# Optimization experiments

Hardware: AMD Instinct MI355X
Metric: run time of the kernel (lower is better)

The kernel has to match this reference:

```python
import jax, jax.numpy as jnp
import numpy as np

D_MODEL = 1024
D_STATE = 16
D_CONV = 4
EXPAND = 2
D_INNER = D_MODEL * EXPAND
B = 2
L = 1024


def setup_inputs() -> dict:
    key = jax.random.key(0)
    ks = jax.random.split(key, 8)
    s = lambda k, shape, scale: jax.random.normal(k, shape, dtype=jnp.float32) * scale
    x = s(ks[0], (B, L, D_MODEL), 1.0)
    W_in = s(ks[1], (2 * D_INNER, D_MODEL), D_MODEL ** -0.5)
    conv_w = s(ks[2], (D_INNER, D_CONV), D_CONV ** -0.5)
    conv_b = s(ks[3], (D_INNER,), 0.02)
    W_x = s(ks[4], (2 * D_STATE + 1, D_INNER), D_INNER ** -0.5)
    dt_w = s(ks[5], (D_INNER, 1), 1.0)
    dt_b = s(ks[6], (D_INNER,), 0.02)
    A_log = jnp.log(jnp.broadcast_to(jnp.arange(1, D_STATE + 1, dtype=jnp.float32), (D_INNER, D_STATE)))
    D_param = jnp.ones((D_INNER,), dtype=jnp.float32)
    W_out = s(ks[7], (D_MODEL, D_INNER), D_INNER ** -0.5)
    return dict(x=x, W_in=W_in, conv_w=conv_w, conv_b=conv_b, W_x=W_x,
                dt_w=dt_w, dt_b=dt_b, A_log=A_log, D_param=D_param, W_out=W_out)


def _causal_dwconv(x, w, b):
    # x: (B,L,D), w: (D,K), b: (D,). torch Conv1d(pad=K-1)[..., :L] == left-pad causal conv.
    K = w.shape[1]
    Lx = x.shape[1]
    xp = jnp.pad(x, ((0, 0), (K - 1, 0), (0, 0)))
    return sum(xp[:, k:k + Lx, :] * w[:, k] for k in range(K)) + b


def reference(x, W_in, conv_w, conv_b, W_x, dt_w, dt_b, A_log, D_param, W_out):
    Bb, Ll, _ = x.shape
    xz = jnp.einsum('bld,ed->ble', x, W_in)          # (B,L,2*D_INNER)
    x_ssm, z = jnp.split(xz, 2, axis=-1)
    xc = jax.nn.silu(_causal_dwconv(x_ssm, conv_w, conv_b))  # (B,L,D_INNER)

    proj = jnp.einsum('bld,ed->ble', xc, W_x)        # (B,L,1+2N)
    dt_raw = proj[..., :1]
    B_vals = proj[..., 1:1 + D_STATE]                # (B,L,N)
    C_vals = proj[..., 1 + D_STATE:]                 # (B,L,N)
    dt = jax.nn.softplus(dt_raw * dt_w[:, 0] + dt_b)  # (B,L,D_INNER)

    A = -jnp.exp(A_log)                              # (D_INNER,N)
    dA = jnp.exp(dt[..., None] * A)                  # (B,L,D,N)
    dBx = dt[..., None] * B_vals[:, :, None, :] * xc[..., None]  # (B,L,D,N)

    def step(h, inputs):
        dA_t, dBx_t, C_t = inputs
        h = dA_t * h + dBx_t                         # (B,D,N)
        y_t = jnp.einsum('bdn,bn->bd', h, C_t)
        return h, y_t

    h0 = jnp.zeros((Bb, D_INNER, D_STATE), dtype=x.dtype)
    xs = (jnp.moveaxis(dA, 1, 0), jnp.moveaxis(dBx, 1, 0), jnp.moveaxis(C_vals, 1, 0))
    _, ys = jax.lax.scan(step, h0, xs)               # ys: (L,B,D)
    y = jnp.moveaxis(ys, 0, 1) + xc * D_param        # skip connection
    y = y * jax.nn.silu(z)
    return jnp.einsum('bld,ed->ble', y, W_out)
```

## Files before the change

kernel.cpp:

```cpp
#include <hip/hip_runtime.h>
#include <cstdint>
#include <cstddef>

#define DM 1024
#define DI 2048
#define DS 16
#define LSEQ 1024
#define NROWS 2048
#define CHUNKS 32
#define CLEN 32
#define PSTRIDE 36

typedef __attribute__((ext_vector_type(8))) short short8;
typedef __attribute__((ext_vector_type(4))) float float4v;

__device__ __forceinline__ float bf2f(ushort u) {
  union { float f; uint32_t i; } v; v.i = ((uint32_t)u) << 16; return v.f;
}
__device__ __forceinline__ ushort f2bf(float f) {
  union { float f; uint32_t i; } v; v.f = f;
  uint32_t x = v.i;
  uint32_t r = (x + 0x7fffu + ((x >> 16) & 1u)) >> 16;
  return (ushort)r;
}

__device__ __forceinline__ void gl2lds16(const ushort* g, ushort* l) {
  __builtin_amdgcn_global_load_lds(
      (const __attribute__((address_space(1))) unsigned int*)g,
      (__attribute__((address_space(3))) unsigned int*)l,
      16, 0, 0);
}

#define NX   (NROWS * DM)
#define NWIN (2 * DI * DM)
#define NWOUT (DM * DI)
#define NWX  (33 * DI)

__global__ __launch_bounds__(256)
void cast_all(const float* __restrict__ x, const float* __restrict__ W_in,
              const float* __restrict__ W_out, const float* __restrict__ Wx,
              ushort* __restrict__ xb, ushort* __restrict__ wib,
              ushort* __restrict__ wob, ushort* __restrict__ wxb) {
  int i = (blockIdx.x * 256 + threadIdx.x) * 8;
  const float* src;
  ushort* dst;
  int off;
  if (i < NX) { src = x; dst = xb; off = 0; }
  else if (i < NX + NWIN) { src = W_in; dst = wib; off = NX; }
  else if (i < NX + NWIN + NWOUT) { src = W_out; dst = wob; off = NX + NWIN; }
  else if (i < NX + NWIN + NWOUT + NWX) { src = Wx; dst = wxb; off = NX + NWIN + NWOUT; }
  else return;
  int j = i - off;
  float4v a = *(const float4v*)(src + j);
  float4v b = *(const float4v*)(src + j + 4);
  short8 o;
#pragma unroll
  for (int k = 0; k < 4; ++k) o[k] = (short)f2bf(a[k]);
#pragma unroll
  for (int k = 0; k < 4; ++k) o[4 + k] = (short)f2bf(b[k]);
  *(short8*)(dst + j) = o;
}

template <typename OUT_T>
__global__ __launch_bounds__(256, 2)
void gemm_bt(const ushort* __restrict__ A, const ushort* __restrict__ B,
             OUT_T* __restrict__ C, int M, int N, int K, int lda, int ldb) {
  __shared__ ushort As[128 * 64];
  __shared__ ushort Bs[128 * 64];
  const int tid = threadIdx.x;
  const int wave = tid >> 6;
  const int lane = tid & 63;
  const int m16 = lane & 15;
  const int quad = lane >> 4;
  const int row0 = blockIdx.x * 128;
  const int col0 = blockIdx.y * 128;
  const int wm = (wave >> 1) * 64;
  const int wn = (wave & 1) * 64;

  const ushort *Ap[4], *Bp[4];
  ushort *Asd[4], *Bsd[4];
#pragma unroll
  for (int q = 0; q < 4; ++q) {
    int c = tid + 256 * q;
    Ap[q] = A + (size_t)(row0 + (c >> 3)) * lda + (c & 7) * 8;
    Bp[q] = B + (size_t)(col0 + (c >> 3)) * ldb + (c & 7) * 8;
    Asd[q] = As + c * 8;
    Bsd[q] = Bs + c * 8;
  }

  float4v acc[4][4] = {};

  for (int k0 = 0; k0 < K; k0 += 64) {
    __syncthreads();
#pragma unroll
    for (int q = 0; q < 4; ++q) gl2lds16(Ap[q], Asd[q]);
#pragma unroll
    for (int q = 0; q < 4; ++q) gl2lds16(Bp[q], Bsd[q]);
#pragma unroll
    for (int q = 0; q < 4; ++q) { Ap[q] += 64; Bp[q] += 64; }
    __syncthreads();

#pragma unroll
    for (int kk = 0; kk < 64; kk += 32) {
      short8 af[4], bfr[4];
#pragma unroll
      for (int i = 0; i < 4; ++i)
        af[i] = *(const short8*)&As[(wm + i * 16 + m16) * 64 + kk + quad * 8];
#pragma unroll
      for (int j = 0; j < 4; ++j)
        bfr[j] = *(const short8*)&Bs[(wn + j * 16 + m16) * 64 + kk + quad * 8];
#pragma unroll
      for (int i = 0; i < 4; ++i)
#pragma unroll
        for (int j = 0; j < 4; ++j)
          acc[i][j] = __builtin_amdgcn_mfma_f32_16x16x32_bf16(af[i], bfr[j], acc[i][j], 0, 0, 0);
    }
  }

#pragma unroll
  for (int i = 0; i < 4; ++i) {
#pragma unroll
    for (int r = 0; r < 4; ++r) {
      int row = row0 + wm + i * 16 + quad * 4 + r;
#pragma unroll
      for (int j = 0; j < 4; ++j) {
        int col = col0 + wn + j * 16 + m16;
        float v = acc[i][j][r];
        if constexpr (sizeof(OUT_T) == 4)
          C[(size_t)row * N + col] = v;
        else
          C[(size_t)row * N + col] = f2bf(v);
      }
    }
  }
}

__global__ __launch_bounds__(256, 2)
void gemm_bt64(const ushort* __restrict__ A, const ushort* __restrict__ B,
               float* __restrict__ C, int M, int N, int K, int lda, int ldb) {
  __shared__ ushort As[64 * 32];
  __shared__ ushort Bs[64 * 32];
  const int tid = threadIdx.x;
  const int wave = tid >> 6;
  const int lane = tid & 63;
  const int m16 = lane & 15;
  const int quad = lane >> 4;
  const int row0 = blockIdx.x * 64;
  const int col0 = blockIdx.y * 64;
  const int wm = (wave >> 1) * 32;
  const int wn = (wave & 1) * 32;

  const int c = tid;
  const ushort* Ap = A + (size_t)(row0 + (c >> 2)) * lda + (c & 3) * 8;
  const ushort* Bp = B + (size_t)(col0 + (c >> 2)) * ldb + (c & 3) * 8;
  ushort* Asd = As + c * 8;
  ushort* Bsd = Bs + c * 8;

  float4v acc[2][2] = {};

  for (int k0 = 0; k0 < K; k0 += 32) {
    __syncthreads();
    gl2lds16(Ap, Asd);
    gl2lds16(Bp, Bsd);
    Ap += 32; Bp += 32;
    __syncthreads();

    short8 af[2], bfr[2];
#pragma unroll
    for (int i = 0; i < 2; ++i)
      af[i] = *(const short8*)&As[(wm + i * 16 + m16) * 32 + quad * 8];
#pragma unroll
    for (int j = 0; j < 2; ++j)
      bfr[j] = *(const short8*)&Bs[(wn + j * 16 + m16) * 32 + quad * 8];
#pragma unroll
    for (int i = 0; i < 2; ++i)
#pragma unroll
      for (int j = 0; j < 2; ++j)
        acc[i][j] = __builtin_amdgcn_mfma_f32_16x16x32_bf16(af[i], bfr[j], acc[i][j], 0, 0, 0);
  }

#pragma unroll
  for (int i = 0; i < 2; ++i) {
#pragma unroll
    for (int r = 0; r < 4; ++r) {
      int row = row0 + wm + i * 16 + quad * 4 + r;
#pragma unroll
      for (int j = 0; j < 2; ++j) {
        int col = col0 + wn + j * 16 + m16;
        C[(size_t)row * N + col] = acc[i][j][r];
      }
    }
  }
}

__global__ __launch_bounds__(256)
void conv_proj_kernel(const ushort* __restrict__ xz,
                      const float* __restrict__ conv_w,
                      const float* __restrict__ conv_b,
                      const ushort* __restrict__ Wx,
                      ushort* __restrict__ xc,
                      float* __restrict__ proj) {
  __shared__ float partial[4][4][33];
  const int row0 = blockIdx.x * 4;
  const int t = threadIdx.x;
  const int lane = t & 63, wave = t >> 6;
  const int d8 = t * 8;

  float w[8][4], bias[8];
#pragma unroll
  for (int j = 0; j < 8; ++j) {
    bias[j] = conv_b[d8 + j];
    float4v wv = *(const float4v*)(conv_w + (d8 + j) * 4);
#pragma unroll
    for (int k = 0; k < 4; ++k) w[j][k] = wv[k];
  }

  float xv[4][8];
#pragma unroll
  for (int rr = 0; rr < 4; ++rr) {
    int row = row0 + rr;
    int l = row & (LSEQ - 1);
    float acc[8];
#pragma unroll
    for (int j = 0; j < 8; ++j) acc[j] = bias[j];
#pragma unroll
    for (int k = 0; k < 4; ++k) {
      int ls = l - 3 + k;
      if (ls >= 0) {
        short8 xr = *(const short8*)(xz + (size_t)(row - 3 + k) * (2 * DI) + d8);
#pragma unroll
        for (int j = 0; j < 8; ++j) acc[j] += bf2f((ushort)xr[j]) * w[j][k];
      }
    }
    short8 o;
#pragma unroll
    for (int j = 0; j < 8; ++j) {
      float v = acc[j];
      v = v / (1.f + __expf(-v));
      xv[rr][j] = v;
      o[j] = (short)f2bf(v);
    }
    *(short8*)(xc + (size_t)row * DI + d8) = o;
  }

  for (int n = 0; n < 33; ++n) {
    short8 w8 = *(const short8*)(Wx + (size_t)n * DI + d8);
    float wv[8];
#pragma unroll
    for (int i = 0; i < 8; ++i) wv[i] = bf2f((ushort)w8[i]);
    float acc[4] = {0.f, 0.f, 0.f, 0.f};
#pragma unroll
    for (int rr = 0; rr < 4; ++rr)
#pragma unroll
      for (int i = 0; i < 8; ++i) acc[rr] += xv[rr][i] * wv[i];
#pragma unroll
    for (int rr = 0; rr < 4; ++rr) {
      acc[rr] += __shfl_xor(acc[rr], 1);
      acc[rr] += __shfl_xor(acc[rr], 2);
      acc[rr] += __shfl_xor(acc[rr], 4);
      acc[rr] += __shfl_xor(acc[rr], 8);
      acc[rr] += __shfl_xor(acc[rr], 16);
      acc[rr] += __shfl_xor(acc[rr], 32);
      if (lane == 0) partial[wave][rr][n] = acc[rr];
    }
  }
  __syncthreads();
  if (t < 33) {
    int col = (t == 0) ? 0 : 3 + t;
#pragma unroll
    for (int rr = 0; rr < 4; ++rr)
      proj[(size_t)(row0 + rr) * PSTRIDE + col] =
          partial[0][rr][t] + partial[1][rr][t] + partial[2][rr][t] + partial[3][rr][t];
  }
}


__global__ __launch_bounds__(256)
void scan_pass1(const float* __restrict__ proj,
                const ushort* __restrict__ xc,
                const float* __restrict__ A_log,
                const float* __restrict__ dt_w,
                const float* __restrict__ dt_b,
                float* __restrict__ aprod,
                float* __restrict__ hend) {
  const int d = blockIdx.x * 256 + threadIdx.x;
  const int ch = blockIdx.y;
  const int b = blockIdx.z;
  float A2[16];
#pragma unroll
  for (int i = 0; i < 4; ++i) {
    float4v a = *(const float4v*)(A_log + (size_t)d * DS + i * 4);
#pragma unroll
    for (int j = 0; j < 4; ++j) A2[i * 4 + j] = -__expf(a[j]) * 1.44269504f;
  }
  const float dtw = dt_w[d], dtb = dt_b[d];
  float h[16];
#pragma unroll
  for (int n = 0; n < 16; ++n) h[n] = 0.f;
  float S = 0.f;
  const size_t rowbase = (size_t)b * LSEQ + ch * CLEN;
#pragma unroll 4
  for (int r = 0; r < CLEN; ++r) {
    const float* pr = proj + (rowbase + r) * PSTRIDE;
    float dtraw = pr[0];
    float4v Bv[4];
#pragma unroll
    for (int i = 0; i < 4; ++i) Bv[i] = *(const float4v*)(pr + 4 + 4 * i);
    float xv = bf2f(xc[(rowbase + r) * DI + d]);
    float draw = dtraw * dtw + dtb;
    float dt = (draw > 20.f) ? draw : __logf(1.f + __expf(draw));
    S += dt;
    float dtx = dt * xv;
#pragma unroll
    for (int n = 0; n < 16; ++n) {
      float dA = exp2f(dt * A2[n]);
      h[n] = dA * h[n] + dtx * Bv[n >> 2][n & 3];
    }
  }
  size_t o = ((size_t)(b * CHUNKS + ch) * DS) * DI + d;
#pragma unroll
  for (int n = 0; n < 16; ++n) {
    aprod[o + (size_t)n * DI] = exp2f(A2[n] * S);
    hend[o + (size_t)n * DI] = h[n];
  }
}

__global__ __launch_bounds__(256)
void scan_pass2(float* __restrict__ aprod, const float* __restrict__ hend) {
  int g = blockIdx.x * 256 + threadIdx.x;
  int d = g & (DI - 1);
  int n = (g >> 11) & 15;
  int b = g >> 15;
  float h = 0.f;
  for (int ch = 0; ch < CHUNKS; ++ch) {
    size_t o = ((size_t)((b * CHUNKS + ch) * DS + n)) * DI + d;
    float a = aprod[o];
    float e = hend[o];
    aprod[o] = h;
    h = a * h + e;
  }
}

__global__ __launch_bounds__(256)
void scan_pass3(const float* __restrict__ proj,
                const ushort* __restrict__ xc,
                const ushort* __restrict__ xz,
                const float* __restrict__ A_log,
                const float* __restrict__ dt_w,
                const float* __restrict__ dt_b,
                const float* __restrict__ D_param,
                const float* __restrict__ hstart,
                ushort* __restrict__ y) {
  const int d = blockIdx.x * 256 + threadIdx.x;
  const int ch = blockIdx.y;
  const int b = blockIdx.z;
  float A2[16];
#pragma unroll
  for (int i = 0; i < 4; ++i) {
    float4v a = *(const float4v*)(A_log + (size_t)d * DS + i * 4);
#pragma unroll
    for (int j = 0; j < 4; ++j) A2[i * 4 + j] = -__expf(a[j]) * 1.44269504f;
  }
  const float dtw = dt_w[d], dtb = dt_b[d];
  const float Dp = D_param[d];
  float h[16];
  size_t o = ((size_t)(b * CHUNKS + ch) * DS) * DI + d;
#pragma unroll
  for (int n = 0; n < 16; ++n) h[n] = hstart[o + (size_t)n * DI];
  const size_t rowbase = (size_t)b * LSEQ + ch * CLEN;
#pragma unroll 4
  for (int r = 0; r < CLEN; ++r) {
    const float* pr = proj + (rowbase + r) * PSTRIDE;
    float dtraw = pr[0];
    float4v Bv[4], Cv[4];
#pragma unroll
    for (int i = 0; i < 4; ++i) Bv[i] = *(const float4v*)(pr + 4 + 4 * i);
#pragma unroll
    for (int i = 0; i < 4; ++i) Cv[i] = *(const float4v*)(pr + 20 + 4 * i);
    float xv = bf2f(xc[(rowbase + r) * DI + d]);
    float zv = bf2f(xz[(rowbase + r) * (2 * DI) + DI + d]);
    float draw = dtraw * dtw + dtb;
    float dt = (draw > 20.f) ? draw : __logf(1.f + __expf(draw));
    float dtx = dt * xv;
    float yv = 0.f;
#pragma unroll
    for (int n = 0; n < 16; ++n) {
      float dA = exp2f(dt * A2[n]);
      h[n] = dA * h[n] + dtx * Bv[n >> 2][n & 3];
      yv += h[n] * Cv[n >> 2][n & 3];
    }
    yv += xv * Dp;
    float sz = zv / (1.f + __expf(-zv));
    y[(rowbase + r) * DI + d] = f2bf(yv * sz);
  }
}

extern "C" void kernel_launch(void* const* d_in, const int* in_sizes, int n_in,
                              void* d_out, int out_size, void* d_ws, size_t ws_size,
                              hipStream_t stream) {
  const float* x       = (const float*)d_in[0];
  const float* W_in    = (const float*)d_in[1];
  const float* conv_w  = (const float*)d_in[2];
  const float* conv_b  = (const float*)d_in[3];
  const float* W_x     = (const float*)d_in[4];
  const float* dt_w    = (const float*)d_in[5];
  const float* dt_b    = (const float*)d_in[6];
  const float* A_log   = (const float*)d_in[7];
  const float* D_param = (const float*)d_in[8];
  const float* W_out   = (const float*)d_in[9];
  float* out = (float*)d_out;

  const size_t MB = 1024 * 1024;
  char* ws = (char*)d_ws;
  ushort* xz    = (ushort*)ws;
  ushort* xc    = (ushort*)(ws + 16 * MB);
  float*  proj  = (float*)(ws + 24 * MB);
  ushort* y     = (ushort*)(ws + 25 * MB);
  ushort* xb    = (ushort*)(ws + 33 * MB);
  ushort* wib   = (ushort*)(ws + 37 * MB);
  float*  aprod = (float*)(ws + 33 * MB);
  float*  hend  = (float*)(ws + 41 * MB);
  ushort* wob   = (ushort*)(ws + 49 * MB);
  ushort* wxb   = (ushort*)(ws + 53 * MB);

  dim3 blk(256);
  cast_all<<<dim3(4129), blk, 0, stream>>>(x, W_in, W_out, W_x, xb, wib, wob, wxb);
  gemm_bt<ushort><<<dim3(16, 32), blk, 0, stream>>>(xb, wib, xz, NROWS, 2 * DI, DM, DM, DM);
  conv_proj_kernel<<<dim3(512), blk, 0, stream>>>(xz, conv_w, conv_b, wxb, xc, proj);
  scan_pass1<<<dim3(8, CHUNKS, 2), blk, 0, stream>>>(proj, xc, A_log, dt_w, dt_b, aprod, hend);
  scan_pass2<<<dim3(256), blk, 0, stream>>>(aprod, hend);
  scan_pass3<<<dim3(8, CHUNKS, 2), blk, 0, stream>>>(proj, xc, xz, A_log, dt_w, dt_b, D_param, aprod, y);
  gemm_bt64<<<dim3(32, 16), blk, 0, stream>>>(y, wob, out, NROWS, DM, DI, DI, DI);
}
```

Baseline: 256.2 us.

## Split conv and x-projection; compute projection with split-K MFMA plus reduce

The fused conv+projection kernel is split into a pure conv/SiLU kernel and a split-K bf16 MFMA GEMM for the 33-wide x projection, with W_x zero-padded to 48 rows, followed by a small reduction kernel that scatters into the proj layout. The aim is to replace the scalar dot products and wave shuffle reductions with matrix-core work spread over more blocks. The cost is two extra kernel launches, a reread of xc from memory, and a partial-sum buffer of 16 slices that must be written and reduced. The projection now also uses bf16 xc instead of fp32 activations.

```diff
diff --git a/kernel.cpp b/kernel.cpp
--- a/kernel.cpp
+++ b/kernel.cpp
@@ -10,6 +10,8 @@
 #define CHUNKS 32
 #define CLEN 32
 #define PSTRIDE 36
+#define NPAD 48
+#define KSPLIT 16
 
 typedef __attribute__((ext_vector_type(8))) short short8;
 typedef __attribute__((ext_vector_type(4))) float float4v;
@@ -35,6 +37,7 @@
 #define NWIN (2 * DI * DM)
 #define NWOUT (DM * DI)
 #define NWX  (33 * DI)
+#define NWXP (NPAD * DI)
 
 __global__ __launch_bounds__(256)
 void cast_all(const float* __restrict__ x, const float* __restrict__ W_in,
@@ -48,8 +51,23 @@
   if (i < NX) { src = x; dst = xb; off = 0; }
   else if (i < NX + NWIN) { src = W_in; dst = wib; off = NX; }
   else if (i < NX + NWIN + NWOUT) { src = W_out; dst = wob; off = NX + NWIN; }
-  else if (i < NX + NWIN + NWOUT + NWX) { src = Wx; dst = wxb; off = NX + NWIN + NWOUT; }
-  else return;
+  else if (i < NX + NWIN + NWOUT + NWXP) {
+    int j = i - (NX + NWIN + NWOUT);
+    short8 o;
+    if (j < NWX) {
+      float4v a = *(const float4v*)(Wx + j);
+      float4v b = *(const float4v*)(Wx + j + 4);
+#pragma unroll
+      for (int k = 0; k < 4; ++k) o[k] = (short)f2bf(a[k]);
+#pragma unroll
+      for (int k = 0; k < 4; ++k) o[4 + k] = (short)f2bf(b[k]);
+    } else {
+#pragma unroll
+      for (int k = 0; k < 8; ++k) o[k] = 0;
+    }
+    *(short8*)(wxb + j) = o;
+    return;
+  } else return;
   int j = i - off;
   float4v a = *(const float4v*)(src + j);
   float4v b = *(const float4v*)(src + j + 4);
@@ -194,84 +212,116 @@
 }
 
 __global__ __launch_bounds__(256)
-void conv_proj_kernel(const ushort* __restrict__ xz,
+void conv_silu_kernel(const ushort* __restrict__ xz,
                       const float* __restrict__ conv_w,
                       const float* __restrict__ conv_b,
-                      const ushort* __restrict__ Wx,
-                      ushort* __restrict__ xc,
-                      float* __restrict__ proj) {
-  __shared__ float partial[4][4][33];
-  const int row0 = blockIdx.x * 4;
-  const int t = threadIdx.x;
-  const int lane = t & 63, wave = t >> 6;
-  const int d8 = t * 8;
-
-  float w[8][4], bias[8];
+                      ushort* __restrict__ xc) {
+  int idx = blockIdx.x * 256 + threadIdx.x;
+  int row = idx >> 8;
+  int d8 = (idx & 255) << 3;
+  int l = row & (LSEQ - 1);
+  float acc[8];
+  float w[8][4];
 #pragma unroll
   for (int j = 0; j < 8; ++j) {
-    bias[j] = conv_b[d8 + j];
+    acc[j] = conv_b[d8 + j];
     float4v wv = *(const float4v*)(conv_w + (d8 + j) * 4);
 #pragma unroll
     for (int k = 0; k < 4; ++k) w[j][k] = wv[k];
   }
-
-  float xv[4][8];
-#pragma unroll
-  for (int rr = 0; rr < 4; ++rr) {
-    int row = row0 + rr;
-    int l = row & (LSEQ - 1);
-    float acc[8];
-#pragma unroll
-    for (int j = 0; j < 8; ++j) acc[j] = bias[j];
-#pragma unroll
-    for (int k = 0; k < 4; ++k) {
-      int ls = l - 3 + k;
-      if (ls >= 0) {
-        short8 xr = *(const short8*)(xz + (size_t)(row - 3 + k) * (2 * DI) + d8);
-#pragma unroll
-        for (int j = 0; j < 8; ++j) acc[j] += bf2f((ushort)xr[j]) * w[j][k];
+#pragma unroll
+  for (int k = 0; k < 4; ++k) {
+    int ls = l - 3 + k;
+    if (ls >= 0) {
+      short8 xr = *(const short8*)(xz + (size_t)(row - 3 + k) * (2 * DI) + d8);
+#pragma unroll
+      for (int j = 0; j < 8; ++j) acc[j] += bf2f((ushort)xr[j]) * w[j][k];
+    }
+  }
+  short8 o;
+#pragma unroll
+  for (int j = 0; j < 8; ++j) {
+    float v = acc[j];
+    v = v / (1.f + __expf(-v));
+    o[j] = (short)f2bf(v);
+  }
+  *(short8*)(xc + (size_t)row * DI + d8) = o;
+}
+
+__global__ __launch_bounds__(256, 2)
+void proj_mfma(const ushort* __restrict__ A, const ushort* __restrict__ B,
+               float* __restrict__ part) {
+  __shared__ ushort As[128 * 32];
+  __shared__ ushort Bs[NPAD * 32];
+  const int tid = threadIdx.x;
+  const int wave = tid >> 6;
+  const int lane = tid & 63;
+  const int m16 = lane & 15;
+  const int quad = lane >> 4;
+  const int row0 = blockIdx.x * 128;
+  const int koff = blockIdx.z * (DI / KSPLIT);
+  const int wm = wave * 32;
+
+  const int c0 = tid, c1 = tid + 256;
+  const ushort* Ap0 = A + (size_t)(row0 + (c0 >> 2)) * DI + koff + (c0 & 3) * 8;
+  const ushort* Ap1 = A + (size_t)(row0 + (c1 >> 2)) * DI + koff + (c1 & 3) * 8;
+  const ushort* Bp0 = B + (size_t)(c0 >> 2) * DI + koff + (c0 & 3) * 8;
+  ushort* Asd0 = As + c0 * 8;
+  ushort* Asd1 = As + c1 * 8;
+  ushort* Bsd0 = Bs + c0 * 8;
+  const bool doB = tid < 192;
+
+  float4v acc[2][3] = {};
+
+#pragma unroll
+  for (int it = 0; it < 4; ++it) {
+    __syncthreads();
+    gl2lds16(Ap0, Asd0);
+    gl2lds16(Ap1, Asd1);
+    if (doB) gl2lds16(Bp0, Bsd0);
+    Ap0 += 32; Ap1 += 32; Bp0 += 32;
+    __syncthreads();
+
+    short8 af[2], bfr[3];
+#pragma unroll
+    for (int i = 0; i < 2; ++i)
+      af[i] = *(const short8*)&As[(wm + i * 16 + m16) * 32 + quad * 8];
+#pragma unroll
+    for (int j = 0; j < 3; ++j)
+      bfr[j] = *(const short8*)&Bs[(j * 16 + m16) * 32 + quad * 8];
+#pragma unroll
+    for (int i = 0; i < 2; ++i)
+#pragma unroll
+      for (int j = 0; j < 3; ++j)
+        acc[i][j] = __builtin_amdgcn_mfma_f32_16x16x32_bf16(af[i], bfr[j], acc[i][j], 0, 0, 0);
+  }
+
+  float* Cp = part + (size_t)blockIdx.z * NROWS * NPAD;
+#pragma unroll
+  for (int i = 0; i < 2; ++i) {
+#pragma unroll
+    for (int r = 0; r < 4; ++r) {
+      int row = row0 + wm + i * 16 + quad * 4 + r;
+#pragma unroll
+      for (int j = 0; j < 3; ++j) {
+        int col = j * 16 + m16;
+        Cp[(size_t)row * NPAD + col] = acc[i][j][r];
       }
     }
-    short8 o;
-#pragma unroll
-    for (int j = 0; j < 8; ++j) {
-      float v = acc[j];
-      v = v / (1.f + __expf(-v));
-      xv[rr][j] = v;
-      o[j] = (short)f2bf(v);
-    }
-    *(short8*)(xc + (size_t)row * DI + d8) = o;
-  }
-
-  for (int n = 0; n < 33; ++n) {
-    short8 w8 = *(const short8*)(Wx + (size_t)n * DI + d8);
-    float wv[8];
-#pragma unroll
-    for (int i = 0; i < 8; ++i) wv[i] = bf2f((ushort)w8[i]);
-    float acc[4] = {0.f, 0.f, 0.f, 0.f};
-#pragma unroll
-    for (int rr = 0; rr < 4; ++rr)
-#pragma unroll
-      for (int i = 0; i < 8; ++i) acc[rr] += xv[rr][i] * wv[i];
-#pragma unroll
-    for (int rr = 0; rr < 4; ++rr) {
-      acc[rr] += __shfl_xor(acc[rr], 1);
-      acc[rr] += __shfl_xor(acc[rr], 2);
-      acc[rr] += __shfl_xor(acc[rr], 4);
-      acc[rr] += __shfl_xor(acc[rr], 8);
-      acc[rr] += __shfl_xor(acc[rr], 16);
-      acc[rr] += __shfl_xor(acc[rr], 32);
-      if (lane == 0) partial[wave][rr][n] = acc[rr];
-    }
-  }
-  __syncthreads();
-  if (t < 33) {
-    int col = (t == 0) ? 0 : 3 + t;
-#pragma unroll
-    for (int rr = 0; rr < 4; ++rr)
-      proj[(size_t)(row0 + rr) * PSTRIDE + col] =
-          partial[0][rr][t] + partial[1][rr][t] + partial[2][rr][t] + partial[3][rr][t];
-  }
+  }
+}
+
+__global__ __launch_bounds__(256)
+void proj_reduce(const float* __restrict__ part, float* __restrict__ proj) {
+  int g = blockIdx.x * 256 + threadIdx.x;
+  if (g >= NROWS * 33) return;
+  int row = g / 33, col = g - row * 33;
+  float s = 0.f;
+#pragma unroll
+  for (int z = 0; z < KSPLIT; ++z)
+    s += part[((size_t)z * NROWS + row) * NPAD + col];
+  int pc = (col == 0) ? 0 : 3 + col;
+  proj[(size_t)row * PSTRIDE + pc] = s;
 }
 
 
@@ -422,11 +472,14 @@
   float*  hend  = (float*)(ws + 41 * MB);
   ushort* wob   = (ushort*)(ws + 49 * MB);
   ushort* wxb   = (ushort*)(ws + 53 * MB);
+  float*  ppart = (float*)(ws + 54 * MB);
 
   dim3 blk(256);
-  cast_all<<<dim3(4129), blk, 0, stream>>>(x, W_in, W_out, W_x, xb, wib, wob, wxb);
+  cast_all<<<dim3(4144), blk, 0, stream>>>(x, W_in, W_out, W_x, xb, wib, wob, wxb);
   gemm_bt<ushort><<<dim3(16, 32), blk, 0, stream>>>(xb, wib, xz, NROWS, 2 * DI, DM, DM, DM);
-  conv_proj_kernel<<<dim3(512), blk, 0, stream>>>(xz, conv_w, conv_b, wxb, xc, proj);
+  conv_silu_kernel<<<dim3(2048), blk, 0, stream>>>(xz, conv_w, conv_b, xc);
+  proj_mfma<<<dim3(16, 1, KSPLIT), blk, 0, stream>>>(xc, wxb, ppart);
+  proj_reduce<<<dim3((NROWS * 33 + 255) / 256), blk, 0, stream>>>(ppart, proj);
   scan_pass1<<<dim3(8, CHUNKS, 2), blk, 0, stream>>>(proj, xc, A_log, dt_w, dt_b, aprod, hend);
   scan_pass2<<<dim3(256), blk, 0, stream>>>(aprod, hend);
   scan_pass3<<<dim3(8, CHUNKS, 2), blk, 0, stream>>>(proj, xc, xz, A_log, dt_w, dt_b, D_param, aprod, y);
```

Result: faster. 235.0 us (-8.3%).
